# Kernel tuning notes

Measured on AMD Instinct MI355X. Metric: run time of the kernel, lower is better.

## Reference

```python
import jax, jax.numpy as jnp
import numpy as np

N_NODES = 100000
N_EDGES = 3200000
C_IN = 128
C_OUT = 64
HEADS = 1
NEG_SLOPE = 0.2  # GraphLayer attention leaky_relu
OUT_SLOPE = 0.01  # nn.LeakyReLU default in GATLayer
BN_EPS = 1e-5


def setup_inputs() -> dict:
    key = jax.random.key(0)
    ks = jax.random.split(key, 12)
    x = jax.random.normal(ks[0], (N_NODES, C_IN), dtype=jnp.float32)
    src = jax.random.randint(ks[1], (N_EDGES,), 0, N_NODES, dtype=jnp.int32)
    # guarantee no self loops so remove_self_loops is a no-op (static shapes)
    off = jax.random.randint(ks[2], (N_EDGES,), 0, N_NODES - 1, dtype=jnp.int32)
    dst = (src + 1 + off) % N_NODES
    edge_index = jnp.stack([src, dst])  # [2, E], row0=src(j), row1=dst(i)
    embedding = jax.random.normal(ks[3], (N_NODES, C_OUT), dtype=jnp.float32)
    lin_w = jax.random.normal(ks[4], (HEADS * C_OUT, C_IN), dtype=jnp.float32) / np.sqrt(C_IN)
    lin_b = jax.random.normal(ks[5], (HEADS * C_OUT,), dtype=jnp.float32) * 0.02
    att_i = jax.random.normal(ks[6], (1, HEADS, C_OUT), dtype=jnp.float32) / np.sqrt(C_OUT)
    att_j = jax.random.normal(ks[7], (1, HEADS, C_OUT), dtype=jnp.float32) / np.sqrt(C_OUT)
    att_em_i = jax.random.normal(ks[8], (1, HEADS, C_OUT), dtype=jnp.float32) / np.sqrt(C_OUT)
    att_em_j = jax.random.normal(ks[9], (1, HEADS, C_OUT), dtype=jnp.float32) / np.sqrt(C_OUT)
    bias = jax.random.normal(ks[10], (C_OUT,), dtype=jnp.float32) * 0.02
    bn_gamma = jax.random.uniform(ks[11], (C_OUT,), dtype=jnp.float32, minval=0.5, maxval=1.5)
    bn_beta = jax.random.normal(jax.random.fold_in(key, 99), (C_OUT,), dtype=jnp.float32) * 0.1
    return {"x": x, "edge_index": edge_index, "embedding": embedding,
            "lin_w": lin_w, "lin_b": lin_b,
            "att_i": att_i, "att_j": att_j,
            "att_em_i": att_em_i, "att_em_j": att_em_j,
            "bias": bias, "bn_gamma": bn_gamma, "bn_beta": bn_beta}


def reference(x, edge_index, embedding, lin_w, lin_b,
              att_i, att_j, att_em_i, att_em_j, bias, bn_gamma, bn_beta):
    N = x.shape[0]
    H, Co = att_i.shape[1], att_i.shape[2]
    node_num = N  # GATLayer passes node_num == number of nodes

    xl = (x @ lin_w.T + lin_b).reshape(N, H, Co)  # lin(x) -> [N,H,Co]

    # add self loops (input edges contain none)
    ar = jnp.arange(N, dtype=edge_index.dtype)
    src = jnp.concatenate([edge_index[0], ar])  # j
    dst = jnp.concatenate([edge_index[1], ar])  # i (target / edge_index_i)

    # per-node attention scores; alpha_e = s_i[dst] + s_j[src]
    # (key_i . cat_att_i) = x_i.att_i + emb_i.att_em_i  -- depends only on node
    emb_h = embedding[:, None, :]  # [N,1,Co] broadcast over heads
    s_i = (xl * att_i).sum(-1) + (emb_h * att_em_i).sum(-1)  # [N,H]
    s_j = (xl * att_j).sum(-1) + (emb_h * att_em_j).sum(-1)  # [N,H]

    emb_idx_i = dst % node_num  # identity here, kept for faithfulness
    emb_idx_j = src % node_num
    alpha = (xl[dst] * att_i).sum(-1) * 0  # placeholder removed below
    alpha = s_i[emb_idx_i] * 0 + s_i[dst] + s_j[src]  # [E,H]
    alpha = jax.nn.leaky_relu(alpha, NEG_SLOPE)

    # segment softmax over target node (dst)
    amax = jax.ops.segment_max(alpha, dst, num_segments=N)  # [N,H]
    ex = jnp.exp(alpha - amax[dst])
    denom = jax.ops.segment_sum(ex, dst, num_segments=N)
    alpha = ex / denom[dst]  # [E,H]

    # weighted messages + scatter-sum aggregate (dropout p=0)
    msg = xl[src] * alpha[:, :, None]  # [E,H,Co]
    agg = jax.ops.segment_sum(msg, dst, num_segments=N)  # [N,H,Co]

    out = agg.mean(axis=1) + bias  # concat=False -> mean over heads, [N,Co]

    # BatchNorm1d (training-mode batch stats, biased variance)
    mu = out.mean(axis=0)
    var = ((out - mu) ** 2).mean(axis=0)
    out = bn_gamma * (out - mu) * jax.lax.rsqrt(var + BN_EPS) + bn_beta
    out = jax.nn.leaky_relu(out, OUT_SLOPE)

    att_weight = alpha[:, :, None]  # [E,H,1], matches returned alpha
    return out, att_weight
```

## Files before the change

### kernel.cpp

```cpp
#include <hip/hip_runtime.h>
#include <hip/hip_bf16.h>

#define CIN 128
#define CO  64

typedef __attribute__((ext_vector_type(8))) short shortx8;
typedef __attribute__((ext_vector_type(4))) float floatx4;

__device__ __forceinline__ float lrelu(float x, float s) { return x > 0.f ? x : x * s; }

__device__ __forceinline__ short f2bs(float f) {
    union { __hip_bfloat16 h; short s; } u;
    u.h = __float2bfloat16(f);
    return u.s;
}

__device__ __forceinline__ shortx8 pack8(const float4& a, const float4& b) {
    shortx8 r;
    r[0] = f2bs(a.x); r[1] = f2bs(a.y); r[2] = f2bs(a.z); r[3] = f2bs(a.w);
    r[4] = f2bs(b.x); r[5] = f2bs(b.y); r[6] = f2bs(b.z); r[7] = f2bs(b.w);
    return r;
}

__global__ __launch_bounds__(256) void k_gemm(
    const float* __restrict__ x, const float* __restrict__ W,
    const float* __restrict__ lb, const float* __restrict__ ai, const float* __restrict__ aj,
    const float* __restrict__ emb, const float* __restrict__ aei, const float* __restrict__ aej,
    __hip_bfloat16* __restrict__ xlb, float* __restrict__ s_i, float* __restrict__ s_j, int N)
{
    __shared__ __hip_bfloat16 tile[4][16 * 72];
    const int lane = threadIdx.x & 63;
    const int wv   = threadIdx.x >> 6;
    const int col0 = lane & 15;
    const int quad = lane >> 4;

    shortx8 wf[4][4];
#pragma unroll
    for (int cg = 0; cg < 4; ++cg)
#pragma unroll
        for (int ks = 0; ks < 4; ++ks) {
            const float* wp = W + (cg * 16 + col0) * CIN + ks * 32 + quad * 8;
            float4 w0 = *(const float4*)wp;
            float4 w1 = *(const float4*)(wp + 4);
            wf[cg][ks] = pack8(w0, w1);
        }
    float biasv[4], aiv[4], ajv[4];
#pragma unroll
    for (int cg = 0; cg < 4; ++cg) {
        biasv[cg] = lb[cg * 16 + col0];
        aiv[cg]   = ai[cg * 16 + col0];
        ajv[cg]   = aj[cg * 16 + col0];
    }
    float4 ei4 = ((const float4*)aei)[col0];
    float4 ej4 = ((const float4*)aej)[col0];

    int tiles = (N + 15) >> 4;
    for (int t = blockIdx.x * 4 + wv; t < tiles; t += gridDim.x * 4) {
        int n0 = t * 16;
        int arow = n0 + col0; if (arow > N - 1) arow = N - 1;
        const float* xp = x + (size_t)arow * CIN + quad * 8;
        float4 a0[4], a1[4];
#pragma unroll
        for (int ks = 0; ks < 4; ++ks) {
            a0[ks] = *(const float4*)(xp + ks * 32);
            a1[ks] = *(const float4*)(xp + ks * 32 + 4);
        }
        floatx4 z = {0.f, 0.f, 0.f, 0.f};
        floatx4 acc[4] = {z, z, z, z};
#pragma unroll
        for (int ks = 0; ks < 4; ++ks) {
            shortx8 af = pack8(a0[ks], a1[ks]);
#pragma unroll
            for (int cg = 0; cg < 4; ++cg)
                acc[cg] = __builtin_amdgcn_mfma_f32_16x16x32_bf16(af, wf[cg][ks], acc[cg], 0, 0, 0);
        }
        float pi[4] = {0, 0, 0, 0}, pj[4] = {0, 0, 0, 0};
        __hip_bfloat16* tp = tile[wv];
#pragma unroll
        for (int cg = 0; cg < 4; ++cg)
#pragma unroll
            for (int r = 0; r < 4; ++r) {
                float v = acc[cg][r] + biasv[cg];
                pi[r] = fmaf(v, aiv[cg], pi[r]);
                pj[r] = fmaf(v, ajv[cg], pj[r]);
                tp[(quad * 4 + r) * 72 + cg * 16 + col0] = __float2bfloat16(v);
            }
#pragma unroll
        for (int r = 0; r < 4; ++r) {
            int nr = n0 + quad * 4 + r; if (nr > N - 1) nr = N - 1;
            float4 e = ((const float4*)(emb + (size_t)nr * CO))[col0];
            pi[r] += e.x * ei4.x + e.y * ei4.y + e.z * ei4.z + e.w * ei4.w;
            pj[r] += e.x * ej4.x + e.y * ej4.y + e.z * ej4.z + e.w * ej4.w;
        }
        __asm__ __volatile__("s_waitcnt lgkmcnt(0)" ::: "memory");
        int rr = lane >> 2, hh = lane & 3;
        int orow = n0 + rr;
        if (orow < N) {
            const float4* sp = (const float4*)(tp + rr * 72 + hh * 16);
            float4 v0 = sp[0], v1 = sp[1];
            float4* gp = (float4*)(xlb + (size_t)orow * CO + hh * 16);
            gp[0] = v0; gp[1] = v1;
        }
#pragma unroll
        for (int r = 0; r < 4; ++r)
#pragma unroll
            for (int off = 1; off < 16; off <<= 1) {
                pi[r] += __shfl_xor(pi[r], off);
                pj[r] += __shfl_xor(pj[r], off);
            }
        if (col0 == 0) {
#pragma unroll
            for (int r = 0; r < 4; ++r) {
                int n = n0 + quad * 4 + r;
                if (n < N) {
                    s_i[n] = pi[r];
                    s_j[n] = pj[r];
                }
            }
        }
    }
}

#define BIN_CHUNK 4096
__global__ __launch_bounds__(512) void k_binA(
    const int* __restrict__ src, const int* __restrict__ dst, int E, int CAP,
    int* __restrict__ gcur, unsigned* __restrict__ ebuf)
{
    __shared__ int hist[1024];
    __shared__ int lscan[1024];
    __shared__ int gofs[1024];
    __shared__ int wsum[8];
    __shared__ int wbase[8];
    __shared__ unsigned sbuf[BIN_CHUNK];
    __shared__ unsigned short sbid[BIN_CHUNK];
    int base = blockIdx.x * BIN_CHUNK;
    int cnt  = min(BIN_CHUNK, E - base);
    int t = threadIdx.x;
    int lane = t & 63, wid = t >> 6;

    hist[2 * t]     = 0;
    hist[2 * t + 1] = 0;
    __syncthreads();
    for (int k = t; k < cnt; k += 512) atomicAdd(&hist[dst[base + k] >> 7], 1);
    __syncthreads();

    int h0 = hist[2 * t], h1 = hist[2 * t + 1];
    int v = h0 + h1;
#pragma unroll
    for (int off = 1; off < 64; off <<= 1) {
        int y = __shfl_up(v, off);
        if (lane >= off) v += y;
    }
    if (lane == 63) wsum[wid] = v;
    __syncthreads();
    if (t == 0) {
        int a = 0;
#pragma unroll
        for (int i = 0; i < 8; ++i) { wbase[i] = a; a += wsum[i]; }
    }
    __syncthreads();
    int excl = v + wbase[wid] - (h0 + h1);
    lscan[2 * t]     = excl;
    lscan[2 * t + 1] = excl + h0;
    __syncthreads();

    for (int b = t; b < 1024; b += 512) {
        int c = hist[b];
        if (c) gofs[b] = b * CAP + atomicAdd(&gcur[b], c) - lscan[b];
        hist[b] = 0;
    }
    __syncthreads();

    for (int k = t; k < cnt; k += 512) {
        int d = dst[base + k];
        int s = src[base + k];
        int b = d >> 7;
        unsigned packed = (unsigned)s | ((unsigned)(d & 127) << 17);
        int loc = lscan[b] + atomicAdd(&hist[b], 1);
        sbuf[loc] = packed;
        sbid[loc] = (unsigned short)b;
    }
    __syncthreads();

    for (int k = t; k < cnt; k += 512) {
        int b = sbid[k];
        ebuf[gofs[b] + k] = sbuf[k];
    }
}

#define CAPMAX 6272
__global__ __launch_bounds__(256) void k_binB(
    const unsigned* __restrict__ ebuf, const int* __restrict__ gcur,
    int2* __restrict__ rowse, int* __restrict__ ssort, int N, int CAP)
{
    __shared__ int h[128];
    __shared__ int sc[128];
    __shared__ int lloc[128];
    __shared__ int lcur[128];
    __shared__ int sbuf[CAPMAX];
    int b = blockIdx.x;
    int start = b << 7;
    int sz = min(128, N - start);
    int eb   = b * CAP;
    int ep0  = b * (CAP + 128);
    int cntB = gcur[b];
    int t = threadIdx.x;
    if (t < 128) { h[t] = 0; lcur[t] = 0; }
    __syncthreads();
    for (int k = t; k < cntB; k += 256) atomicAdd(&h[ebuf[eb + k] >> 17], 1);
    __syncthreads();
    if (t < 128) sc[t] = h[t];
    __syncthreads();
    for (int off = 1; off < 128; off <<= 1) {
        int y = (t >= off && t < 128) ? sc[t - off] : 0;
        __syncthreads();
        if (t < 128) sc[t] += y;
        __syncthreads();
    }
    if (t < sz) {
        int l = (sc[t] - h[t]) + t;
        lloc[t] = l;
        rowse[start + t] = make_int2(ep0 + l, h[t] + 1);
        sbuf[l + h[t]] = start + t;
    }
    __syncthreads();
    for (int k = t; k < cntB; k += 256) {
        unsigned e = ebuf[eb + k];
        int doff = (int)(e >> 17);
        int s    = (int)(e & 0x1FFFFu);
        int p = atomicAdd(&lcur[doff], 1);
        sbuf[lloc[doff] + p] = s;
    }
    __syncthreads();
    int tot = cntB + sz;
    for (int k = t; k < tot; k += 256)
        ssort[ep0 + k] = sbuf[k];
}

__global__ __launch_bounds__(256) void k_agg(
    const __hip_bfloat16* __restrict__ xlb,
    const float* __restrict__ s_i, const float* __restrict__ s_j,
    const int2* __restrict__ rowse, const int* __restrict__ ssort,
    const float* __restrict__ bias, int N,
    float* __restrict__ outp, float2* __restrict__ pd,
    float* __restrict__ spread)
{
    __shared__ float r1s[4][64];
    __shared__ float r2s[4][64];
    int lane = threadIdx.x & 63;
    int wv   = threadIdx.x >> 6;
    int n    = blockIdx.x * 4 + wv;
    int grp  = lane >> 3;
    int q    = lane & 7;

    float acc[8] = {0, 0, 0, 0, 0, 0, 0, 0};
    float den = 0.f;
    float val[8] = {0, 0, 0, 0, 0, 0, 0, 0};

    if (n < N) {
        int2 se = rowse[n];
        int r0 = se.x, cnt = se.y;
        float si_n = s_i[n];
        const int* sp = ssort + r0;
        const unsigned short* xb = (const unsigned short*)xlb;

        auto GATHER = [&](int s) -> uint4 {
            return *(const uint4*)(xb + ((size_t)s << 6) + (q << 3));
        };
        auto PROC = [&](float w, uint4 g) {
            den += w;
            acc[0] = fmaf(w, __uint_as_float(g.x << 16),          acc[0]);
            acc[1] = fmaf(w, __uint_as_float(g.x & 0xffff0000u),  acc[1]);
            acc[2] = fmaf(w, __uint_as_float(g.y << 16),          acc[2]);
            acc[3] = fmaf(w, __uint_as_float(g.y & 0xffff0000u),  acc[3]);
            acc[4] = fmaf(w, __uint_as_float(g.z << 16),          acc[4]);
            acc[5] = fmaf(w, __uint_as_float(g.z & 0xffff0000u),  acc[5]);
            acc[6] = fmaf(w, __uint_as_float(g.w << 16),          acc[6]);
            acc[7] = fmaf(w, __uint_as_float(g.w & 0xffff0000u),  acc[7]);
        };

        int cnt8 = cnt & ~7;
        if (cnt8 > 0) {
            int   s_c  = sp[grp];
            uint4 g_c  = GATHER(s_c);
            float sj_c = s_j[s_c];
            int k = 0;
            for (; k + 16 <= cnt8; k += 8) {
                int   s_n  = sp[k + 8 + grp];
                uint4 g_n  = GATHER(s_n);
                float sj_n = s_j[s_n];
                float a = si_n + sj_c;
                PROC(__expf(a > 0.f ? a : 0.2f * a), g_c);
                g_c = g_n; sj_c = sj_n;
            }
            float a = si_n + sj_c;
            PROC(__expf(a > 0.f ? a : 0.2f * a), g_c);
        }
        for (int idx = cnt8 + grp; idx < cnt; idx += 8) {
            int s = sp[idx];
            float sj = s_j[s];
            uint4 g = GATHER(s);
            float a = si_n + sj;
            PROC(__expf(a > 0.f ? a : 0.2f * a), g);
        }

#pragma unroll
        for (int j = 0; j < 8; ++j) {
            acc[j] += __shfl_xor(acc[j], 8);
            acc[j] += __shfl_xor(acc[j], 16);
            acc[j] += __shfl_xor(acc[j], 32);
        }
        den += __shfl_xor(den, 8);
        den += __shfl_xor(den, 16);
        den += __shfl_xor(den, 32);

        float inv = 1.0f / den;
#pragma unroll
        for (int j = 0; j < 8; ++j)
            val[j] = acc[j] * inv + bias[q * 8 + j];

        if (grp == 0) {
            float4 v0 = make_float4(val[0], val[1], val[2], val[3]);
            float4 v1 = make_float4(val[4], val[5], val[6], val[7]);
            float* op = outp + (size_t)n * CO + q * 8;
            ((float4*)op)[0] = v0;
            ((float4*)op)[1] = v1;
        }
        if (lane == 0) pd[n] = make_float2(si_n, inv);
    }
    if (grp == 0) {
#pragma unroll
        for (int j = 0; j < 8; ++j) {
            r1s[wv][q * 8 + j] = val[j];
            r2s[wv][q * 8 + j] = val[j] * val[j];
        }
    }
    __syncthreads();
    if (threadIdx.x < 64) {
        int l = threadIdx.x;
        float s1 = r1s[0][l] + r1s[1][l] + r1s[2][l] + r1s[3][l];
        float s2 = r2s[0][l] + r2s[1][l] + r2s[2][l] + r2s[3][l];
        int slot = blockIdx.x & 255;
        atomicAdd(&spread[slot * 128 + l],      s1);
        atomicAdd(&spread[slot * 128 + 64 + l], s2);
    }
}

__global__ __launch_bounds__(512) void k_fat2(
    const int* __restrict__ src, const int* __restrict__ dst, int E, int N,
    const float2* __restrict__ pd, const float* __restrict__ s_j,
    float* __restrict__ att,
    const float* __restrict__ spread, const float* __restrict__ gamma,
    const float* __restrict__ beta, float* __restrict__ scale, float* __restrict__ shift)
{
    __shared__ float red[4][128];
    __shared__ float tot[128];
    if (blockIdx.x == 0) {
        int c = threadIdx.x & 127;
        int p = threadIdx.x >> 7;
        float a = 0.f;
        for (int s = p; s < 256; s += 4) a += spread[s * 128 + c];
        red[p][c] = a;
        __syncthreads();
        if (threadIdx.x < 128) {
            float t = 0.f;
#pragma unroll
            for (int q = 0; q < 4; ++q) t += red[q][c];
            tot[c] = t;
        }
        __syncthreads();
        if (threadIdx.x < 64) {
            float inv = 1.f / (float)N;
            float mu  = tot[threadIdx.x] * inv;
            float msq = tot[64 + threadIdx.x] * inv;
            float var = msq - mu * mu;
            float sc  = gamma[threadIdx.x] * rsqrtf(var + 1e-5f);
            scale[threadIdx.x] = sc;
            shift[threadIdx.x] = beta[threadIdx.x] - mu * sc;
        }
        return;
    }
    int i = (blockIdx.x - 1) * 512 + threadIdx.x;
    int tot_e = E + N;
    if (i >= tot_e) return;
    int s, d;
    if (i < E) { s = src[i]; d = dst[i]; } else { s = d = i - E; }
    float2 p = pd[d];
    float a = lrelu(p.x + s_j[s], 0.2f);
    att[i] = __expf(a) * p.y;
}

__global__ void k_bnapply(float* __restrict__ outp, int N,
                          const float* __restrict__ scale, const float* __restrict__ shift)
{
    int i = blockIdx.x * 256 + threadIdx.x;
    int tot = N * CO / 4;
    if (i >= tot) return;
    float4 v = ((float4*)outp)[i];
    int c0 = (i * 4) & (CO - 1);
    v.x = lrelu(fmaf(scale[c0 + 0], v.x, shift[c0 + 0]), 0.01f);
    v.y = lrelu(fmaf(scale[c0 + 1], v.y, shift[c0 + 1]), 0.01f);
    v.z = lrelu(fmaf(scale[c0 + 2], v.z, shift[c0 + 2]), 0.01f);
    v.w = lrelu(fmaf(scale[c0 + 3], v.w, shift[c0 + 3]), 0.01f);
    ((float4*)outp)[i] = v;
}

extern "C" void kernel_launch(void* const* d_in, const int* in_sizes, int n_in,
                              void* d_out, int out_size, void* d_ws, size_t ws_size,
                              hipStream_t stream)
{
    const float* x    = (const float*)d_in[0];
    const int*   ei   = (const int*)  d_in[1];
    const float* emb  = (const float*)d_in[2];
    const float* W    = (const float*)d_in[3];
    const float* lb   = (const float*)d_in[4];
    const float* ai   = (const float*)d_in[5];
    const float* aj   = (const float*)d_in[6];
    const float* aei  = (const float*)d_in[7];
    const float* aej  = (const float*)d_in[8];
    const float* bias = (const float*)d_in[9];
    const float* gam  = (const float*)d_in[10];
    const float* bet  = (const float*)d_in[11];

    int N = in_sizes[0] / CIN;
    int E = in_sizes[1] / 2;
    const int* srcv = ei;
    const int* dstv = ei + E;
    int NBUK = (N + 127) >> 7;

    int avg = (E + NBUK - 1) / NBUK;
    int CAP = ((avg * 3 / 2) + 255) & ~255;
    if (CAP + 128 > CAPMAX) CAP = CAPMAX - 128;

    float* ws = (float*)d_ws;
    size_t o = 0;
    __hip_bfloat16* xlb = (__hip_bfloat16*)(ws + o); o += (size_t)N * CO / 2;
    float* s_i   = ws + o; o += N;
    float* s_j   = ws + o; o += N;
    float2* pd   = (float2*)(ws + o); o += 2 * (size_t)N;
    int2*  rowse = (int2*)(ws + o); o += 2 * (size_t)N;
    size_t zoff  = o;
    int*   gcur  = (int*)(ws + o); o += 1024;
    float* spread= ws + o;         o += 256 * 128;
    size_t zbytes = (o - zoff) * sizeof(float);
    float* scale = ws + o; o += CO;
    float* shift = ws + o; o += CO;
    unsigned* ebuf = (unsigned*)(ws + o); o += (size_t)NBUK * CAP;
    int*   ssort = (int*)(ws + o); o += (size_t)NBUK * (CAP + 128) + 64;

    float* out_nodes = (float*)d_out;
    float* out_att   = out_nodes + (size_t)N * CO;

    hipMemsetAsync((void*)gcur, 0, zbytes, stream);

    int CHB = (E + BIN_CHUNK - 1) / BIN_CHUNK;
    k_gemm<<<512, 256, 0, stream>>>(x, W, lb, ai, aj, emb, aei, aej, xlb, s_i, s_j, N);
    k_binA<<<CHB, 512, 0, stream>>>(srcv, dstv, E, CAP, gcur, ebuf);
    k_binB<<<NBUK, 256, 0, stream>>>(ebuf, gcur, rowse, ssort, N, CAP);
    k_agg<<<(N + 3) / 4, 256, 0, stream>>>(xlb, s_i, s_j, rowse, ssort, bias, N,
                                           out_nodes, pd, spread);
    k_fat2<<<1 + (E + N + 511) / 512, 512, 0, stream>>>(srcv, dstv, E, N, pd, s_j,
                                                        out_att, spread, gam, bet,
                                                        scale, shift);
    k_bnapply<<<((N * CO / 4) + 255) / 256, 256, 0, stream>>>(out_nodes, N, scale, shift);
}
```

Before: 316.5 us.

## Fuse bucket sort into aggregation kernel, keeping sorted sources in shared memory

Merges the per-bucket counting sort (k_binB) with the attention-weighted aggregation (k_agg) into one kernel, k_aggB. Sorted source indices stay in LDS instead of going through a global ssort/rowse round trip. Each 512-thread block handles one 128-node bucket, with each wave processing 16 nodes one after another and accumulating BatchNorm partial sums in registers. The change also doubles the binning chunk size and triples the GEMM grid. The trade-off is fewer, larger blocks with serialized per-wave node loops, which may hide gather latency less well.

```diff
diff --git a/kernel.cpp b/kernel.cpp
--- a/kernel.cpp
+++ b/kernel.cpp
@@ -121,7 +121,7 @@
     }
 }
 
-#define BIN_CHUNK 4096
+#define BIN_CHUNK 8192
 __global__ __launch_bounds__(512) void k_binA(
     const int* __restrict__ src, const int* __restrict__ dst, int E, int CAP,
     int* __restrict__ gcur, unsigned* __restrict__ ebuf)
@@ -189,25 +189,32 @@
 }
 
 #define CAPMAX 6272
-__global__ __launch_bounds__(256) void k_binB(
+__global__ __launch_bounds__(512) void k_aggB(
+    const __hip_bfloat16* __restrict__ xlb,
+    const float* __restrict__ s_i, const float* __restrict__ s_j,
     const unsigned* __restrict__ ebuf, const int* __restrict__ gcur,
-    int2* __restrict__ rowse, int* __restrict__ ssort, int N, int CAP)
+    const float* __restrict__ bias, int N, int CAP,
+    float* __restrict__ outp, float2* __restrict__ pd,
+    float* __restrict__ spread)
 {
     __shared__ int h[128];
     __shared__ int sc[128];
     __shared__ int lloc[128];
     __shared__ int lcur[128];
     __shared__ int sbuf[CAPMAX];
+    __shared__ float r1s[8][64];
+    __shared__ float r2s[8][64];
+
     int b = blockIdx.x;
     int start = b << 7;
     int sz = min(128, N - start);
     int eb   = b * CAP;
-    int ep0  = b * (CAP + 128);
     int cntB = gcur[b];
     int t = threadIdx.x;
+
     if (t < 128) { h[t] = 0; lcur[t] = 0; }
     __syncthreads();
-    for (int k = t; k < cntB; k += 256) atomicAdd(&h[ebuf[eb + k] >> 17], 1);
+    for (int k = t; k < cntB; k += 512) atomicAdd(&h[ebuf[eb + k] >> 17], 1);
     __syncthreads();
     if (t < 128) sc[t] = h[t];
     __syncthreads();
@@ -220,11 +227,10 @@
     if (t < sz) {
         int l = (sc[t] - h[t]) + t;
         lloc[t] = l;
-        rowse[start + t] = make_int2(ep0 + l, h[t] + 1);
         sbuf[l + h[t]] = start + t;
     }
     __syncthreads();
-    for (int k = t; k < cntB; k += 256) {
+    for (int k = t; k < cntB; k += 512) {
         unsigned e = ebuf[eb + k];
         int doff = (int)(e >> 17);
         int s    = (int)(e & 0x1FFFFu);
@@ -232,37 +238,26 @@
         sbuf[lloc[doff] + p] = s;
     }
     __syncthreads();
-    int tot = cntB + sz;
-    for (int k = t; k < tot; k += 256)
-        ssort[ep0 + k] = sbuf[k];
-}
-
-__global__ __launch_bounds__(256) void k_agg(
-    const __hip_bfloat16* __restrict__ xlb,
-    const float* __restrict__ s_i, const float* __restrict__ s_j,
-    const int2* __restrict__ rowse, const int* __restrict__ ssort,
-    const float* __restrict__ bias, int N,
-    float* __restrict__ outp, float2* __restrict__ pd,
-    float* __restrict__ spread)
-{
-    __shared__ float r1s[4][64];
-    __shared__ float r2s[4][64];
-    int lane = threadIdx.x & 63;
-    int wv   = threadIdx.x >> 6;
-    int n    = blockIdx.x * 4 + wv;
+
+    int lane = t & 63;
+    int wv   = t >> 6;
     int grp  = lane >> 3;
     int q    = lane & 7;
-
-    float acc[8] = {0, 0, 0, 0, 0, 0, 0, 0};
-    float den = 0.f;
-    float val[8] = {0, 0, 0, 0, 0, 0, 0, 0};
-
-    if (n < N) {
-        int2 se = rowse[n];
-        int r0 = se.x, cnt = se.y;
+    const unsigned short* xb = (const unsigned short*)xlb;
+
+    float vsum[8] = {0, 0, 0, 0, 0, 0, 0, 0};
+    float vsq[8]  = {0, 0, 0, 0, 0, 0, 0, 0};
+
+    for (int i = 0; i < 16; ++i) {
+        int tl = wv * 16 + i;
+        if (tl >= sz) break;
+        int n   = start + tl;
+        int loc = lloc[tl];
+        int cnt = h[tl] + 1;
         float si_n = s_i[n];
-        const int* sp = ssort + r0;
-        const unsigned short* xb = (const unsigned short*)xlb;
+
+        float acc[8] = {0, 0, 0, 0, 0, 0, 0, 0};
+        float den = 0.f;
 
         auto GATHER = [&](int s) -> uint4 {
             return *(const uint4*)(xb + ((size_t)s << 6) + (q << 3));
@@ -281,12 +276,12 @@
 
         int cnt8 = cnt & ~7;
         if (cnt8 > 0) {
-            int   s_c  = sp[grp];
+            int   s_c  = sbuf[loc + grp];
             uint4 g_c  = GATHER(s_c);
             float sj_c = s_j[s_c];
             int k = 0;
             for (; k + 16 <= cnt8; k += 8) {
-                int   s_n  = sp[k + 8 + grp];
+                int   s_n  = sbuf[loc + k + 8 + grp];
                 uint4 g_n  = GATHER(s_n);
                 float sj_n = s_j[s_n];
                 float a = si_n + sj_c;
@@ -297,7 +292,7 @@
             PROC(__expf(a > 0.f ? a : 0.2f * a), g_c);
         }
         for (int idx = cnt8 + grp; idx < cnt; idx += 8) {
-            int s = sp[idx];
+            int s = sbuf[loc + idx];
             float sj = s_j[s];
             uint4 g = GATHER(s);
             float a = si_n + sj;
@@ -315,9 +310,13 @@
         den += __shfl_xor(den, 32);
 
         float inv = 1.0f / den;
-#pragma unroll
-        for (int j = 0; j < 8; ++j)
+        float val[8];
+#pragma unroll
+        for (int j = 0; j < 8; ++j) {
             val[j] = acc[j] * inv + bias[q * 8 + j];
+            vsum[j] += val[j];
+            vsq[j]  += val[j] * val[j];
+        }
 
         if (grp == 0) {
             float4 v0 = make_float4(val[0], val[1], val[2], val[3]);
@@ -328,21 +327,22 @@
         }
         if (lane == 0) pd[n] = make_float2(si_n, inv);
     }
+
     if (grp == 0) {
 #pragma unroll
         for (int j = 0; j < 8; ++j) {
-            r1s[wv][q * 8 + j] = val[j];
-            r2s[wv][q * 8 + j] = val[j] * val[j];
-        }
-    }
-    __syncthreads();
-    if (threadIdx.x < 64) {
-        int l = threadIdx.x;
-        float s1 = r1s[0][l] + r1s[1][l] + r1s[2][l] + r1s[3][l];
-        float s2 = r2s[0][l] + r2s[1][l] + r2s[2][l] + r2s[3][l];
-        int slot = blockIdx.x & 255;
-        atomicAdd(&spread[slot * 128 + l],      s1);
-        atomicAdd(&spread[slot * 128 + 64 + l], s2);
+            r1s[wv][q * 8 + j] = vsum[j];
+            r2s[wv][q * 8 + j] = vsq[j];
+        }
+    }
+    __syncthreads();
+    if (t < 64) {
+        float s1 = 0.f, s2 = 0.f;
+#pragma unroll
+        for (int w = 0; w < 8; ++w) { s1 += r1s[w][t]; s2 += r2s[w][t]; }
+        int slot = b & 255;
+        atomicAdd(&spread[slot * 128 + t],      s1);
+        atomicAdd(&spread[slot * 128 + 64 + t], s2);
     }
 }
 
@@ -438,7 +438,6 @@
     float* s_i   = ws + o; o += N;
     float* s_j   = ws + o; o += N;
     float2* pd   = (float2*)(ws + o); o += 2 * (size_t)N;
-    int2*  rowse = (int2*)(ws + o); o += 2 * (size_t)N;
     size_t zoff  = o;
     int*   gcur  = (int*)(ws + o); o += 1024;
     float* spread= ws + o;         o += 256 * 128;
@@ -446,7 +445,6 @@
     float* scale = ws + o; o += CO;
     float* shift = ws + o; o += CO;
     unsigned* ebuf = (unsigned*)(ws + o); o += (size_t)NBUK * CAP;
-    int*   ssort = (int*)(ws + o); o += (size_t)NBUK * (CAP + 128) + 64;
 
     float* out_nodes = (float*)d_out;
     float* out_att   = out_nodes + (size_t)N * CO;
@@ -454,11 +452,10 @@
     hipMemsetAsync((void*)gcur, 0, zbytes, stream);
 
     int CHB = (E + BIN_CHUNK - 1) / BIN_CHUNK;
-    k_gemm<<<512, 256, 0, stream>>>(x, W, lb, ai, aj, emb, aei, aej, xlb, s_i, s_j, N);
+    k_gemm<<<1536, 256, 0, stream>>>(x, W, lb, ai, aj, emb, aei, aej, xlb, s_i, s_j, N);
     k_binA<<<CHB, 512, 0, stream>>>(srcv, dstv, E, CAP, gcur, ebuf);
-    k_binB<<<NBUK, 256, 0, stream>>>(ebuf, gcur, rowse, ssort, N, CAP);
-    k_agg<<<(N + 3) / 4, 256, 0, stream>>>(xlb, s_i, s_j, rowse, ssort, bias, N,
-                                           out_nodes, pd, spread);
+    k_aggB<<<NBUK, 512, 0, stream>>>(xlb, s_i, s_j, ebuf, gcur, bias, N, CAP,
+                                     out_nodes, pd, spread);
     k_fat2<<<1 + (E + N + 511) / 512, 512, 0, stream>>>(srcv, dstv, E, N, pd, s_j,
                                                         out_att, spread, gam, bet,
                                                         scale, shift);
```

Measured after the change: 331.3 us. 4.7% more time.
